# Optimization experiments

Hardware: AMD Instinct MI355X
Metric: run time of the kernel (lower is better)

The kernel has to match this reference:

```python
import jax, jax.numpy as jnp
import numpy as np

B = 16          # number of point clouds
N_COARSE = 1024  # points per cloud at coarse level
N_FINE = 4096    # points per cloud at fine level
C_IN = 256       # coarse feature channels
C_SKIP = 128     # fine skip feature channels
C_HID = 256
EPS = 1e-16


def setup_inputs() -> dict:
    key = jax.random.key(0)
    ks = jax.random.split(key, 8)
    x = jax.random.normal(ks[0], (B * N_COARSE, C_IN), dtype=jnp.float32)
    pos = jax.random.uniform(ks[1], (B * N_COARSE, 3), dtype=jnp.float32)
    x_skip = jax.random.normal(ks[2], (B * N_FINE, C_SKIP), dtype=jnp.float32)
    pos_skip = jax.random.uniform(ks[3], (B * N_FINE, 3), dtype=jnp.float32)
    # uniform batch assignment (sorted), one segment per cloud
    batch = jnp.repeat(jnp.arange(B, dtype=jnp.int32), N_COARSE)
    batch_skip = jnp.repeat(jnp.arange(B, dtype=jnp.int32), N_FINE)
    # MLP params: Linear(384 -> 256) + ReLU, Linear(256 -> 256) + ReLU
    c0 = C_IN + C_SKIP
    W1 = jax.random.normal(ks[4], (c0, C_HID), dtype=jnp.float32) / np.sqrt(c0)
    b1 = jnp.zeros((C_HID,), dtype=jnp.float32)
    W2 = jax.random.normal(ks[5], (C_HID, C_HID), dtype=jnp.float32) / np.sqrt(C_HID)
    b2 = jnp.zeros((C_HID,), dtype=jnp.float32)
    return {"x": x, "pos": pos, "x_skip": x_skip, "pos_skip": pos_skip,
            "W1": W1, "b1": b1, "W2": W2, "b2": b2,
            "batch": batch, "batch_skip": batch_skip, "k": 3}


def _knn_interpolate(x, pos, pos_skip, k):
    # batch is uniform: reshape into [B, n, ...] blocks (same as per-batch kNN)
    xb = x.reshape(B, N_COARSE, -1)          # [B, Nc, C]
    pc = pos.reshape(B, N_COARSE, 3)         # [B, Nc, 3]
    pf = pos_skip.reshape(B, N_FINE, 3)      # [B, Nf, 3]
    # squared pairwise distances within each cloud: [B, Nf, Nc]
    d2 = jnp.sum((pf[:, :, None, :] - pc[:, None, :, :]) ** 2, axis=-1)
    neg_d2, idx = jax.lax.top_k(-d2, k)      # k nearest -> [B, Nf, k]
    w = 1.0 / jnp.maximum(-neg_d2, EPS)      # inverse-squared-distance weights
    gathered = jax.vmap(lambda xc, i: xc[i])(xb, idx)  # [B, Nf, k, C]
    interp = jnp.sum(w[..., None] * gathered, axis=2) / jnp.sum(w, axis=2, keepdims=True)
    return interp.reshape(B * N_FINE, -1)    # [B*Nf, C]


def reference(x, pos, x_skip, pos_skip, W1, b1, W2, b2, batch, batch_skip, k):
    x_up = _knn_interpolate(x, pos, pos_skip, k)
    h = jnp.concatenate([x_up, x_skip], axis=1)          # [B*Nf, C_IN+C_SKIP]
    h = jax.nn.relu(h @ W1 + b1)
    h = jax.nn.relu(h @ W2 + b2)
    return (h, pos_skip, batch_skip)
```

## Files before the change

kernel.cpp:

```cpp
#include <hip/hip_runtime.h>

#define B_ 16
#define NC 1024
#define NF 4096
#define CIN 256
#define CSKIP 128
#define CHID 256
#define MTOT (B_ * NF)
#define EPS_ 1e-16f

typedef _Float16 f16;
typedef __attribute__((ext_vector_type(8))) _Float16 f16x8;
typedef __attribute__((ext_vector_type(4))) _Float16 f16x4;
typedef __attribute__((ext_vector_type(4))) float f32x4;


__global__ __launch_bounds__(256) void misc_kernel(
    const float* __restrict__ pos, const float* __restrict__ pos_skip,
    const int* __restrict__ batch_skip,
    const float* __restrict__ W1, const float* __restrict__ W2,
    const float* __restrict__ b1,
    int* __restrict__ idx3, float* __restrict__ w3,
    f16* __restrict__ W1aT, f16* __restrict__ W1bT, f16* __restrict__ W2T,
    float* __restrict__ b1p, float* __restrict__ out_tail)
{
    __shared__ float4 cpos[NC];
    __shared__ float  cd[32 * 24];
    __shared__ int    ci[32 * 24];

    const int bid = blockIdx.x;
    if (bid < 2048) {
        const int b  = bid >> 7;
        const int fb = bid & 127;
        const float* cp = pos + (size_t)b * NC * 3;
        for (int i = threadIdx.x; i < NC; i += 256)
            cpos[i] = make_float4(cp[i * 3], cp[i * 3 + 1], cp[i * 3 + 2], 0.0f);
        __syncthreads();

        const int fl = threadIdx.x & 31;
        const int q  = threadIdx.x >> 5;
        const int f  = b * NF + fb * 32 + fl;
        const float px = pos_skip[f * 3 + 0];
        const float py = pos_skip[f * 3 + 1];
        const float pz = pos_skip[f * 3 + 2];

        float d0 = 3.4e38f, d1 = 3.4e38f, d2 = 3.4e38f;
        int   i0 = 0, i1 = 0, i2 = 0;
        const int jbase = q << 7;
#pragma unroll 4
        for (int jj = 0; jj < 128; ++jj) {
            const int j = jbase + jj;
            float4 c = cpos[j];
            float dx = px - c.x, dy = py - c.y, dz = pz - c.z;
            float d = fmaf(dx, dx, fmaf(dy, dy, dz * dz));
            const bool c2 = d < d2, c1 = d < d1, c0 = d < d0;
            d2 = c1 ? d1 : (c2 ? d : d2);  i2 = c1 ? i1 : (c2 ? j : i2);
            d1 = c0 ? d0 : (c1 ? d : d1);  i1 = c0 ? i0 : (c1 ? j : i1);
            d0 = c0 ? d  : d0;             i0 = c0 ? j  : i0;
        }
        const int cb = fl * 24 + q * 3;
        cd[cb + 0] = d0; cd[cb + 1] = d1; cd[cb + 2] = d2;
        ci[cb + 0] = i0; ci[cb + 1] = i1; ci[cb + 2] = i2;
        __syncthreads();

        if (threadIdx.x < 32) {
            float e0 = 3.4e38f, e1 = 3.4e38f, e2 = 3.4e38f;
            int   j0 = 0, j1 = 0, j2 = 0;
#pragma unroll
            for (int s = 0; s < 24; ++s) {
                const float d = cd[fl * 24 + s];
                const int   j = ci[fl * 24 + s];
                const bool c2 = d < e2, c1 = d < e1, c0 = d < e0;
                e2 = c1 ? e1 : (c2 ? d : e2);  j2 = c1 ? j1 : (c2 ? j : j2);
                e1 = c0 ? e0 : (c1 ? d : e1);  j1 = c0 ? j0 : (c1 ? j : j1);
                e0 = c0 ? d  : e0;             j0 = c0 ? j  : j0;
            }
            const float w0 = 1.0f / fmaxf(e0, EPS_);
            const float w1 = 1.0f / fmaxf(e1, EPS_);
            const float w2 = 1.0f / fmaxf(e2, EPS_);
            const float inv = 1.0f / (w0 + w1 + w2);
            idx3[f * 3 + 0] = b * NC + j0;
            idx3[f * 3 + 1] = b * NC + j1;
            idx3[f * 3 + 2] = b * NC + j2;
            w3[f * 3 + 0] = w0 * inv;
            w3[f * 3 + 1] = w1 * inv;
            w3[f * 3 + 2] = w2 * inv;
        }
    } else if (bid < 2689) {
        const int t = (bid - 2048) * 256 + threadIdx.x;
        if (t < 256 * 256) {
            const int k = t >> 8, n = t & 255;
            W1aT[n * 256 + k] = (f16)W1[k * 256 + n];
        } else if (t < 256 * 256 + 128 * 256) {
            const int u = t - 256 * 256;
            const int k = u >> 8, n = u & 255;
            W1bT[n * 128 + k] = (f16)W1[(256 + k) * 256 + n];
        } else if (t < 256 * 256 + 128 * 256 + 256 * 256) {
            const int u = t - 256 * 256 - 128 * 256;
            const int n = u >> 8, j = u & 255;
            const int k = (j & ~63) + ((j & 3) << 4) + ((j >> 2) & 15);
            W2T[n * 256 + j] = (f16)W2[k * 256 + n];
        } else if (t < 256 * 256 + 128 * 256 + 256 * 256 + 256) {
            const int j = t - (256 * 256 + 128 * 256 + 256 * 256);
            const int k = (j & ~63) + ((j & 3) << 4) + ((j >> 2) & 15);
            b1p[j] = b1[k];
        }
    } else {
        const int i = (bid - 2689) * 256 + threadIdx.x;
        const int npos = MTOT * 3;
        if (i < npos)               out_tail[i] = pos_skip[i];
        else if (i < npos + MTOT)   out_tail[i] = (float)batch_skip[i - npos];
    }
}

__device__ __forceinline__ void gload16(const void* g, void* l)
{
    __builtin_amdgcn_global_load_lds(
        (const __attribute__((address_space(1))) unsigned int*)g,
        (__attribute__((address_space(3))) unsigned int*)l, 16, 0, 0);
}

__global__ __launch_bounds__(256, 2) void gemm_y(
    const float* __restrict__ A, const f16* __restrict__ Bt,
    f16* __restrict__ C)
{
    __shared__ f16 As[128 * 64];
    __shared__ f16 Bs[256 * 64];
    const int tid  = threadIdx.x;
    const int lane = tid & 63;
    const int wid  = tid >> 6;
    const int wr   = wid >> 1, wc = wid & 1;
    const int m0   = blockIdx.x * 128;

    const int srow = tid >> 1;
    const int scg  = tid & 1;
    const int srow_l = lane >> 3;
    const int kch    = (lane & 7) ^ ((lane >> 3) & 7);

    f32x4 acc[4][8] = {};

    for (int k0 = 0; k0 < 256; k0 += 64) {
#pragma unroll
        for (int r = 0; r < 8; ++r) {
            const int c = (wid << 3) + r;
            const int row = (c << 3) + srow_l;
            gload16(Bt + (size_t)row * 256 + k0 + kch * 8,
                    (char*)Bs + (c << 10));
        }
        {
            const float* p = A + (size_t)(m0 + srow) * 256 + k0 + scg * 32;
            float v[32];
#pragma unroll
            for (int j = 0; j < 8; ++j) {
                float4 a = ((const float4*)p)[j];
                v[j * 4 + 0] = a.x; v[j * 4 + 1] = a.y;
                v[j * 4 + 2] = a.z; v[j * 4 + 3] = a.w;
            }
#pragma unroll
            for (int j = 0; j < 4; ++j) {
                f16x8 hh;
#pragma unroll
                for (int t2 = 0; t2 < 8; ++t2) hh[t2] = (f16)v[j * 8 + t2];
                const int sphys = (scg * 4 + j) ^ (srow & 7);
                *(f16x8*)((char*)As + srow * 128 + sphys * 16) = hh;
            }
        }
        __syncthreads();

#pragma unroll
        for (int h = 0; h < 2; ++h) {
            f16x8 aF[4];
#pragma unroll
            for (int m = 0; m < 4; ++m) {
                const int row  = wr * 64 + m * 16 + (lane & 15);
                const int kg   = (h << 2) + (lane >> 4);
                const int slot = kg ^ (row & 7);
                aF[m] = *(const f16x8*)((const char*)As + row * 128 + slot * 16);
            }
#pragma unroll
            for (int n = 0; n < 8; ++n) {
                const int row  = wc * 128 + n * 16 + (lane & 15);
                const int kg   = (h << 2) + (lane >> 4);
                const int slot = kg ^ (row & 7);
                f16x8 bF = *(const f16x8*)((const char*)Bs + row * 128 + slot * 16);
#pragma unroll
                for (int m = 0; m < 4; ++m)
                    acc[m][n] = __builtin_amdgcn_mfma_f32_16x16x32_f16(
                        aF[m], bF, acc[m][n], 0, 0, 0);
            }
        }
        __syncthreads();
    }

    const int qq = lane & 15;
#pragma unroll
    for (int m = 0; m < 4; ++m) {
        const int rb = wr * 64 + m * 16 + ((lane >> 4) << 2);
#pragma unroll
        for (int r = 0; r < 4; ++r) {
            const int rg = m0 + rb + r;
#pragma unroll
            for (int g = 0; g < 2; ++g) {
                f16x4 hv;
#pragma unroll
                for (int n = 0; n < 4; ++n)
                    hv[n] = (f16)acc[m][g * 4 + n][r];
                *(f16x4*)&C[(size_t)rg * 256 + wc * 128 + g * 64 + qq * 4] = hv;
            }
        }
    }
}

__global__ __launch_bounds__(256, 2) void gemm1b_fused(
    const float* __restrict__ A, const f16* __restrict__ Bt,
    const f16* __restrict__ y,
    const int* __restrict__ idx3, const float* __restrict__ w3,
    const float* __restrict__ b1p, f16* __restrict__ h1)
{
    __shared__ f16 As[128 * 64];
    __shared__ f16 Bs[256 * 64];
    const int tid  = threadIdx.x;
    const int lane = tid & 63;
    const int wid  = tid >> 6;
    const int wr   = wid >> 1, wc = wid & 1;
    const int m0   = blockIdx.x * 128;

    const int srow = tid >> 1;
    const int scg  = tid & 1;
    const int srow_l = lane >> 3;
    const int kch    = (lane & 7) ^ ((lane >> 3) & 7);

    f32x4 acc[4][8] = {};

    for (int k0 = 0; k0 < 128; k0 += 64) {
#pragma unroll
        for (int r = 0; r < 8; ++r) {
            const int c = (wid << 3) + r;
            const int row = (c << 3) + srow_l;
            gload16(Bt + (size_t)row * 128 + k0 + kch * 8,
                    (char*)Bs + (c << 10));
        }
        {
            const float* p = A + (size_t)(m0 + srow) * 128 + k0 + scg * 32;
            float v[32];
#pragma unroll
            for (int j = 0; j < 8; ++j) {
                float4 a = ((const float4*)p)[j];
                v[j * 4 + 0] = a.x; v[j * 4 + 1] = a.y;
                v[j * 4 + 2] = a.z; v[j * 4 + 3] = a.w;
            }
#pragma unroll
            for (int j = 0; j < 4; ++j) {
                f16x8 hh;
#pragma unroll
                for (int t2 = 0; t2 < 8; ++t2) hh[t2] = (f16)v[j * 8 + t2];
                const int sphys = (scg * 4 + j) ^ (srow & 7);
                *(f16x8*)((char*)As + srow * 128 + sphys * 16) = hh;
            }
        }
        __syncthreads();

#pragma unroll
        for (int h = 0; h < 2; ++h) {
            f16x8 aF[4];
#pragma unroll
            for (int m = 0; m < 4; ++m) {
                const int row  = wr * 64 + m * 16 + (lane & 15);
                const int kg   = (h << 2) + (lane >> 4);
                const int slot = kg ^ (row & 7);
                aF[m] = *(const f16x8*)((const char*)As + row * 128 + slot * 16);
            }
#pragma unroll
            for (int n = 0; n < 8; ++n) {
                const int row  = wc * 128 + n * 16 + (lane & 15);
                const int kg   = (h << 2) + (lane >> 4);
                const int slot = kg ^ (row & 7);
                f16x8 bF = *(const f16x8*)((const char*)Bs + row * 128 + slot * 16);
#pragma unroll
                for (int m = 0; m < 4; ++m)
                    acc[m][n] = __builtin_amdgcn_mfma_f32_16x16x32_f16(
                        aF[m], bF, acc[m][n], 0, 0, 0);
            }
        }
        __syncthreads();
    }

    const int qq = lane & 15;
    const f32x4 bv0 = *(const f32x4*)&b1p[wc * 128 + qq * 4];
    const f32x4 bv1 = *(const f32x4*)&b1p[wc * 128 + 64 + qq * 4];
#pragma unroll
    for (int m = 0; m < 4; ++m) {
        const int rb = wr * 64 + m * 16 + ((lane >> 4) << 2);
#pragma unroll
        for (int r = 0; r < 4; ++r) {
            const int rg = m0 + rb + r;
            const int i0 = idx3[rg * 3 + 0], i1 = idx3[rg * 3 + 1], i2 = idx3[rg * 3 + 2];
            const float w0 = w3[rg * 3 + 0], w1 = w3[rg * 3 + 1], w2 = w3[rg * 3 + 2];
#pragma unroll
            for (int g = 0; g < 2; ++g) {
                const int jb = wc * 128 + g * 64 + qq * 4;
                f16x4 y0 = *(const f16x4*)&y[(size_t)i0 * 256 + jb];
                f16x4 y1 = *(const f16x4*)&y[(size_t)i1 * 256 + jb];
                f16x4 y2 = *(const f16x4*)&y[(size_t)i2 * 256 + jb];
                const f32x4 bv = g ? bv1 : bv0;
                f16x4 hv;
#pragma unroll
                for (int n = 0; n < 4; ++n) {
                    float v = acc[m][g * 4 + n][r]
                            + w0 * (float)y0[n] + w1 * (float)y1[n] + w2 * (float)y2[n]
                            + bv[n];
                    hv[n] = (f16)fmaxf(v, 0.0f);
                }
                *(f16x4*)&h1[(size_t)rg * 256 + jb] = hv;
            }
        }
    }
}

__global__ __launch_bounds__(256, 2) void gemm2_kernel(
    const f16* __restrict__ A, const f16* __restrict__ Bt,
    const float* __restrict__ bias, float* __restrict__ out)
{
    __shared__ f16 As[128 * 64];
    __shared__ f16 Bs[256 * 64];
    const int tid  = threadIdx.x;
    const int lane = tid & 63;
    const int wid  = tid >> 6;
    const int wr   = wid >> 1, wc = wid & 1;
    const int m0   = blockIdx.x * 128;

    const int srow_l = lane >> 3;
    const int kch    = (lane & 7) ^ ((lane >> 3) & 7);

    f32x4 acc[4][8] = {};

    for (int k0 = 0; k0 < 256; k0 += 64) {
#pragma unroll
        for (int r = 0; r < 4; ++r) {
            const int c = (wid << 2) + r;
            const int row = (c << 3) + srow_l;
            gload16(A + (size_t)(m0 + row) * 256 + k0 + kch * 8,
                    (char*)As + (c << 10));
        }
#pragma unroll
        for (int r = 0; r < 8; ++r) {
            const int c = (wid << 3) + r;
            const int row = (c << 3) + srow_l;
            gload16(Bt + (size_t)row * 256 + k0 + kch * 8,
                    (char*)Bs + (c << 10));
        }
        __syncthreads();

#pragma unroll
        for (int h = 0; h < 2; ++h) {
            f16x8 aF[4];
#pragma unroll
            for (int m = 0; m < 4; ++m) {
                const int row  = wr * 64 + m * 16 + (lane & 15);
                const int kg   = (h << 2) + (lane >> 4);
                const int slot = kg ^ (row & 7);
                aF[m] = *(const f16x8*)((const char*)As + row * 128 + slot * 16);
            }
#pragma unroll
            for (int n = 0; n < 8; ++n) {
                const int row  = wc * 128 + n * 16 + (lane & 15);
                const int kg   = (h << 2) + (lane >> 4);
                const int slot = kg ^ (row & 7);
                f16x8 bF = *(const f16x8*)((const char*)Bs + row * 128 + slot * 16);
#pragma unroll
                for (int m = 0; m < 4; ++m)
                    acc[m][n] = __builtin_amdgcn_mfma_f32_16x16x32_f16(
                        aF[m], bF, acc[m][n], 0, 0, 0);
            }
        }
        __syncthreads();
    }

#pragma unroll
    for (int m = 0; m < 4; ++m) {
#pragma unroll
        for (int n = 0; n < 8; ++n) {
            const int col = wc * 128 + n * 16 + (lane & 15);
            const float bv = bias[col];
#pragma unroll
            for (int r = 0; r < 4; ++r) {
                const int row = m0 + wr * 64 + m * 16 + ((lane >> 4) << 2) + r;
                out[(size_t)row * 256 + col] = fmaxf(acc[m][n][r] + bv, 0.0f);
            }
        }
    }
}

extern "C" void kernel_launch(void* const* d_in, const int* in_sizes, int n_in,
                              void* d_out, int out_size, void* d_ws, size_t ws_size,
                              hipStream_t stream)
{
    const float* x        = (const float*)d_in[0];
    const float* pos      = (const float*)d_in[1];
    const float* x_skip   = (const float*)d_in[2];
    const float* pos_skip = (const float*)d_in[3];
    const float* W1       = (const float*)d_in[4];
    const float* b1       = (const float*)d_in[5];
    const float* W2       = (const float*)d_in[6];
    const float* b2       = (const float*)d_in[7];
    const int*   batch_skip = (const int*)d_in[9];
    float* out = (float*)d_out;

    char* ws = (char*)d_ws;
    int*   idx3  = (int*)ws;
    float* w3    = (float*)(ws + (1u << 20));
    f16*   W1aT  = (f16*)(ws + (2u << 20));
    f16*   W1bT  = (f16*)(ws + (2u << 20) + (256u << 10));
    f16*   W2T   = (f16*)(ws + (2u << 20) + (512u << 10));
    float* b1p   = (float*)(ws + (2u << 20) + (768u << 10));
    f16*   y     = (f16*)(ws + (4u << 20));
    f16*   h1    = (f16*)(ws + (16u << 20));

    misc_kernel<<<3713, 256, 0, stream>>>(
        pos, pos_skip, batch_skip, W1, W2, b1,
        idx3, w3, W1aT, W1bT, W2T, b1p, out + (size_t)MTOT * CHID);

    gemm_y<<<B_ * NC / 128, 256, 0, stream>>>(x, W1aT, y);

    gemm1b_fused<<<MTOT / 128, 256, 0, stream>>>(x_skip, W1bT, y, idx3, w3, b1p, h1);

    gemm2_kernel<<<MTOT / 128, 256, 0, stream>>>(h1, W2T, b2, out);
}
```

Measured before the change: 198.5 us.

## Fuse GEMM1b and GEMM2 via LDS-resident h1; fold y GEMM into misc kernel

```diff
diff --git a/kernel.cpp b/kernel.cpp
--- a/kernel.cpp
+++ b/kernel.cpp
@@ -15,34 +15,137 @@
 typedef __attribute__((ext_vector_type(4))) float f32x4;
 
 
-__global__ __launch_bounds__(256) void misc_kernel(
+__device__ __forceinline__ void gload16(const void* g, void* l)
+{
+    __builtin_amdgcn_global_load_lds(
+        (const __attribute__((address_space(1))) unsigned int*)g,
+        (__attribute__((address_space(3))) unsigned int*)l, 16, 0, 0);
+}
+
+__global__ __launch_bounds__(256, 4) void misc_kernel(
+    const float* __restrict__ x,
     const float* __restrict__ pos, const float* __restrict__ pos_skip,
     const int* __restrict__ batch_skip,
     const float* __restrict__ W1, const float* __restrict__ W2,
     const float* __restrict__ b1,
     int* __restrict__ idx3, float* __restrict__ w3,
-    f16* __restrict__ W1aT, f16* __restrict__ W1bT, f16* __restrict__ W2T,
-    float* __restrict__ b1p, float* __restrict__ out_tail)
+    f16* __restrict__ W1bT, f16* __restrict__ W2T, float* __restrict__ b1p,
+    f16* __restrict__ y, float* __restrict__ out_tail)
 {
-    __shared__ float4 cpos[NC];
-    __shared__ float  cd[32 * 24];
-    __shared__ int    ci[32 * 24];
-
+    __shared__ __align__(16) char smem[32768];
     const int bid = blockIdx.x;
-    if (bid < 2048) {
-        const int b  = bid >> 7;
-        const int fb = bid & 127;
+
+    if (bid < 256) {
+        f16* As = (f16*)smem;
+        f16* Bs = (f16*)(smem + 16384);
+        const int m0 = (bid >> 1) * 128;
+        const int n0 = (bid & 1) * 128;
+        const int tid  = threadIdx.x;
+        const int lane = tid & 63;
+        const int wid  = tid >> 6;
+        const int wr   = wid >> 1, wc = wid & 1;
+        const int srow = tid >> 1;
+        const int scg  = tid & 1;
+        const int bn4  = (tid & 31) << 2;
+        const int bkb  = (tid >> 5) << 3;
+
+        f32x4 acc[4][4] = {};
+        for (int k0 = 0; k0 < 256; k0 += 64) {
+            {
+                const float* p = x + (size_t)(m0 + srow) * 256 + k0 + scg * 32;
+                float v[32];
+#pragma unroll
+                for (int j = 0; j < 8; ++j) {
+                    float4 a = ((const float4*)p)[j];
+                    v[j*4+0]=a.x; v[j*4+1]=a.y; v[j*4+2]=a.z; v[j*4+3]=a.w;
+                }
+#pragma unroll
+                for (int j = 0; j < 4; ++j) {
+                    f16x8 hh;
+#pragma unroll
+                    for (int t2 = 0; t2 < 8; ++t2) hh[t2] = (f16)v[j*8+t2];
+                    const int sphys = (scg*4 + j) ^ (srow & 7);
+                    *(f16x8*)((char*)As + srow*128 + sphys*16) = hh;
+                }
+            }
+#pragma unroll
+            for (int c = 0; c < 2; ++c) {
+                const int k = bkb + c * 4;
+                const float* wp = W1 + (size_t)(k0 + k) * 256 + n0 + bn4;
+                float4 r0 = *(const float4*)(wp);
+                float4 r1 = *(const float4*)(wp + 256);
+                float4 r2 = *(const float4*)(wp + 512);
+                float4 r3 = *(const float4*)(wp + 768);
+                const int half  = (k >> 2) & 1;
+                const int kslot = k >> 3;
+                f16x4 t0, t1, t2v, t3;
+                t0[0]=(f16)r0.x; t0[1]=(f16)r1.x; t0[2]=(f16)r2.x; t0[3]=(f16)r3.x;
+                t1[0]=(f16)r0.y; t1[1]=(f16)r1.y; t1[2]=(f16)r2.y; t1[3]=(f16)r3.y;
+                t2v[0]=(f16)r0.z; t2v[1]=(f16)r1.z; t2v[2]=(f16)r2.z; t2v[3]=(f16)r3.z;
+                t3[0]=(f16)r0.w; t3[1]=(f16)r1.w; t3[2]=(f16)r2.w; t3[3]=(f16)r3.w;
+                *(f16x4*)((char*)Bs + (bn4+0)*128 + ((kslot ^ ((bn4+0)&7))*16) + half*8) = t0;
+                *(f16x4*)((char*)Bs + (bn4+1)*128 + ((kslot ^ ((bn4+1)&7))*16) + half*8) = t1;
+                *(f16x4*)((char*)Bs + (bn4+2)*128 + ((kslot ^ ((bn4+2)&7))*16) + half*8) = t2v;
+                *(f16x4*)((char*)Bs + (bn4+3)*128 + ((kslot ^ ((bn4+3)&7))*16) + half*8) = t3;
+            }
+            __syncthreads();
+#pragma unroll
+            for (int h = 0; h < 2; ++h) {
+                f16x8 aF[4], bF[4];
+#pragma unroll
+                for (int m = 0; m < 4; ++m) {
+                    const int row  = wr*64 + m*16 + (lane & 15);
+                    const int kg   = (h<<2) + (lane>>4);
+                    const int slot = kg ^ (row & 7);
+                    aF[m] = *(const f16x8*)((const char*)As + row*128 + slot*16);
+                }
+#pragma unroll
+                for (int n = 0; n < 4; ++n) {
+                    const int row  = wc*64 + n*16 + (lane & 15);
+                    const int kg   = (h<<2) + (lane>>4);
+                    const int slot = kg ^ (row & 7);
+                    bF[n] = *(const f16x8*)((const char*)Bs + row*128 + slot*16);
+                }
+#pragma unroll
+                for (int m = 0; m < 4; ++m)
+#pragma unroll
+                    for (int n = 0; n < 4; ++n)
+                        acc[m][n] = __builtin_amdgcn_mfma_f32_16x16x32_f16(
+                            aF[m], bF[n], acc[m][n], 0, 0, 0);
+            }
+            __syncthreads();
+        }
+        const int qq = lane & 15;
+#pragma unroll
+        for (int m = 0; m < 4; ++m) {
+            const int rb = wr*64 + m*16 + ((lane>>4) << 2);
+#pragma unroll
+            for (int r = 0; r < 4; ++r) {
+                const int rg = m0 + rb + r;
+                f16x4 hv;
+#pragma unroll
+                for (int n = 0; n < 4; ++n) hv[n] = (f16)acc[m][n][r];
+                *(f16x4*)&y[(size_t)rg * 256 + n0 + wc*64 + qq*4] = hv;
+            }
+        }
+    } else if (bid < 2304) {
+        float4* cpos = (float4*)smem;
+        float*  cd   = (float*)(smem + 16384);
+        int*    ci   = (int*)(smem + 19456);
+        const int kb = bid - 256;
+        const int b  = kb >> 7;
+        const int fb = kb & 127;
         const float* cp = pos + (size_t)b * NC * 3;
         for (int i = threadIdx.x; i < NC; i += 256)
-            cpos[i] = make_float4(cp[i * 3], cp[i * 3 + 1], cp[i * 3 + 2], 0.0f);
+            cpos[i] = make_float4(cp[i*3], cp[i*3+1], cp[i*3+2], 0.0f);
         __syncthreads();
 
         const int fl = threadIdx.x & 31;
         const int q  = threadIdx.x >> 5;
         const int f  = b * NF + fb * 32 + fl;
-        const float px = pos_skip[f * 3 + 0];
-        const float py = pos_skip[f * 3 + 1];
-        const float pz = pos_skip[f * 3 + 2];
+        const float px = pos_skip[f*3+0];
+        const float py = pos_skip[f*3+1];
+        const float pz = pos_skip[f*3+2];
 
         float d0 = 3.4e38f, d1 = 3.4e38f, d2 = 3.4e38f;
         int   i0 = 0, i1 = 0, i2 = 0;
@@ -59,8 +162,8 @@
             d0 = c0 ? d  : d0;             i0 = c0 ? j  : i0;
         }
         const int cb = fl * 24 + q * 3;
-        cd[cb + 0] = d0; cd[cb + 1] = d1; cd[cb + 2] = d2;
-        ci[cb + 0] = i0; ci[cb + 1] = i1; ci[cb + 2] = i2;
+        cd[cb+0] = d0; cd[cb+1] = d1; cd[cb+2] = d2;
+        ci[cb+0] = i0; ci[cb+1] = i1; ci[cb+2] = i2;
         __syncthreads();
 
         if (threadIdx.x < 32) {
@@ -68,8 +171,8 @@
             int   j0 = 0, j1 = 0, j2 = 0;
 #pragma unroll
             for (int s = 0; s < 24; ++s) {
-                const float d = cd[fl * 24 + s];
-                const int   j = ci[fl * 24 + s];
+                const float d = cd[fl*24 + s];
+                const int   j = ci[fl*24 + s];
                 const bool c2 = d < e2, c1 = d < e1, c0 = d < e0;
                 e2 = c1 ? e1 : (c2 ? d : e2);  j2 = c1 ? j1 : (c2 ? j : j2);
                 e1 = c0 ? e0 : (c1 ? d : e1);  j1 = c0 ? j0 : (c1 ? j : j1);
@@ -79,29 +182,25 @@
             const float w1 = 1.0f / fmaxf(e1, EPS_);
             const float w2 = 1.0f / fmaxf(e2, EPS_);
             const float inv = 1.0f / (w0 + w1 + w2);
-            idx3[f * 3 + 0] = b * NC + j0;
-            idx3[f * 3 + 1] = b * NC + j1;
-            idx3[f * 3 + 2] = b * NC + j2;
-            w3[f * 3 + 0] = w0 * inv;
-            w3[f * 3 + 1] = w1 * inv;
-            w3[f * 3 + 2] = w2 * inv;
+            idx3[f*3+0] = b * NC + j0;
+            idx3[f*3+1] = b * NC + j1;
+            idx3[f*3+2] = b * NC + j2;
+            w3[f*3+0] = w0 * inv;
+            w3[f*3+1] = w1 * inv;
+            w3[f*3+2] = w2 * inv;
         }
     } else if (bid < 2689) {
-        const int t = (bid - 2048) * 256 + threadIdx.x;
-        if (t < 256 * 256) {
+        const int t = (bid - 2304) * 256 + threadIdx.x;
+        if (t < 128 * 256) {
             const int k = t >> 8, n = t & 255;
-            W1aT[n * 256 + k] = (f16)W1[k * 256 + n];
-        } else if (t < 256 * 256 + 128 * 256) {
-            const int u = t - 256 * 256;
-            const int k = u >> 8, n = u & 255;
             W1bT[n * 128 + k] = (f16)W1[(256 + k) * 256 + n];
-        } else if (t < 256 * 256 + 128 * 256 + 256 * 256) {
-            const int u = t - 256 * 256 - 128 * 256;
+        } else if (t < 128 * 256 + 256 * 256) {
+            const int u = t - 128 * 256;
             const int n = u >> 8, j = u & 255;
             const int k = (j & ~63) + ((j & 3) << 4) + ((j >> 2) & 15);
             W2T[n * 256 + j] = (f16)W2[k * 256 + n];
-        } else if (t < 256 * 256 + 128 * 256 + 256 * 256 + 256) {
-            const int j = t - (256 * 256 + 128 * 256 + 256 * 256);
+        } else if (t < 128 * 256 + 256 * 256 + 256) {
+            const int j = t - (128 * 256 + 256 * 256);
             const int k = (j & ~63) + ((j & 3) << 4) + ((j >> 2) & 15);
             b1p[j] = b1[k];
         }
@@ -113,78 +212,75 @@
     }
 }
 
-__device__ __forceinline__ void gload16(const void* g, void* l)
+__global__ __launch_bounds__(256, 2) void fused_gemm12(
+    const float* __restrict__ A,
+    const f16* __restrict__ B1t,
+    const f16* __restrict__ y,
+    const int* __restrict__ idx3, const float* __restrict__ w3,
+    const float* __restrict__ b1p,
+    const f16* __restrict__ B2t,
+    const float* __restrict__ b2,
+    float* __restrict__ out)
 {
-    __builtin_amdgcn_global_load_lds(
-        (const __attribute__((address_space(1))) unsigned int*)g,
-        (__attribute__((address_space(3))) unsigned int*)l, 16, 0, 0);
-}
-
-__global__ __launch_bounds__(256, 2) void gemm_y(
-    const float* __restrict__ A, const f16* __restrict__ Bt,
-    f16* __restrict__ C)
-{
-    __shared__ f16 As[128 * 64];
-    __shared__ f16 Bs[256 * 64];
+    __shared__ __align__(16) char lds[65536];
+    f16*  Bs  = (f16*)lds;
+    f16*  As  = (f16*)(lds + 32768);
+    char* h1s = lds + 32768;
+
     const int tid  = threadIdx.x;
     const int lane = tid & 63;
     const int wid  = tid >> 6;
     const int wr   = wid >> 1, wc = wid & 1;
-    const int m0   = blockIdx.x * 128;
-
-    const int srow = tid >> 1;
-    const int scg  = tid & 1;
+    const int m0   = blockIdx.x * 64;
+
     const int srow_l = lane >> 3;
     const int kch    = (lane & 7) ^ ((lane >> 3) & 7);
 
-    f32x4 acc[4][8] = {};
-
-    for (int k0 = 0; k0 < 256; k0 += 64) {
+    f32x4 acc[2][8] = {};
+    for (int k0 = 0; k0 < 128; k0 += 64) {
 #pragma unroll
         for (int r = 0; r < 8; ++r) {
             const int c = (wid << 3) + r;
             const int row = (c << 3) + srow_l;
-            gload16(Bt + (size_t)row * 256 + k0 + kch * 8,
-                    (char*)Bs + (c << 10));
+            gload16(B1t + (size_t)row * 128 + k0 + kch * 8, (char*)Bs + (c << 10));
         }
         {
-            const float* p = A + (size_t)(m0 + srow) * 256 + k0 + scg * 32;
-            float v[32];
-#pragma unroll
-            for (int j = 0; j < 8; ++j) {
+            const int arow = tid >> 2, acg = tid & 3;
+            const float* p = A + (size_t)(m0 + arow) * 128 + k0 + acg * 16;
+            float v[16];
+#pragma unroll
+            for (int j = 0; j < 4; ++j) {
                 float4 a = ((const float4*)p)[j];
-                v[j * 4 + 0] = a.x; v[j * 4 + 1] = a.y;
-                v[j * 4 + 2] = a.z; v[j * 4 + 3] = a.w;
-            }
-#pragma unroll
-            for (int j = 0; j < 4; ++j) {
+                v[j*4+0]=a.x; v[j*4+1]=a.y; v[j*4+2]=a.z; v[j*4+3]=a.w;
+            }
+#pragma unroll
+            for (int j = 0; j < 2; ++j) {
                 f16x8 hh;
 #pragma unroll
-                for (int t2 = 0; t2 < 8; ++t2) hh[t2] = (f16)v[j * 8 + t2];
-                const int sphys = (scg * 4 + j) ^ (srow & 7);
-                *(f16x8*)((char*)As + srow * 128 + sphys * 16) = hh;
-            }
-        }
-        __syncthreads();
-
+                for (int t2 = 0; t2 < 8; ++t2) hh[t2] = (f16)v[j*8+t2];
+                const int sphys = (acg*2 + j) ^ (arow & 7);
+                *(f16x8*)((char*)As + arow*128 + sphys*16) = hh;
+            }
+        }
+        __syncthreads();
 #pragma unroll
         for (int h = 0; h < 2; ++h) {
-            f16x8 aF[4];
-#pragma unroll
-            for (int m = 0; m < 4; ++m) {
-                const int row  = wr * 64 + m * 16 + (lane & 15);
-                const int kg   = (h << 2) + (lane >> 4);
+            f16x8 aF[2];
+#pragma unroll
+            for (int m = 0; m < 2; ++m) {
+                const int row  = wr*32 + m*16 + (lane & 15);
+                const int kg   = (h<<2) + (lane>>4);
                 const int slot = kg ^ (row & 7);
-                aF[m] = *(const f16x8*)((const char*)As + row * 128 + slot * 16);
+                aF[m] = *(const f16x8*)((const char*)As + row*128 + slot*16);
             }
 #pragma unroll
             for (int n = 0; n < 8; ++n) {
-                const int row  = wc * 128 + n * 16 + (lane & 15);
-                const int kg   = (h << 2) + (lane >> 4);
+                const int row  = wc*128 + n*16 + (lane & 15);
+                const int kg   = (h<<2) + (lane>>4);
                 const int slot = kg ^ (row & 7);
-                f16x8 bF = *(const f16x8*)((const char*)Bs + row * 128 + slot * 16);
-#pragma unroll
-                for (int m = 0; m < 4; ++m)
+                f16x8 bF = *(const f16x8*)((const char*)Bs + row*128 + slot*16);
+#pragma unroll
+                for (int m = 0; m < 2; ++m)
                     acc[m][n] = __builtin_amdgcn_mfma_f32_16x16x32_f16(
                         aF[m], bF, acc[m][n], 0, 0, 0);
             }
@@ -193,112 +289,20 @@
     }
 
     const int qq = lane & 15;
-#pragma unroll
-    for (int m = 0; m < 4; ++m) {
-        const int rb = wr * 64 + m * 16 + ((lane >> 4) << 2);
+    const f32x4 bv0 = *(const f32x4*)&b1p[wc*128 + qq*4];
+    const f32x4 bv1 = *(const f32x4*)&b1p[wc*128 + 64 + qq*4];
+#pragma unroll
+    for (int m = 0; m < 2; ++m) {
+        const int rb = wr*32 + m*16 + ((lane>>4) << 2);
 #pragma unroll
         for (int r = 0; r < 4; ++r) {
-            const int rg = m0 + rb + r;
+            const int rl = rb + r;
+            const int rg = m0 + rl;
+            const int i0 = idx3[rg*3+0], i1 = idx3[rg*3+1], i2 = idx3[rg*3+2];
+            const float w0 = w3[rg*3+0], w1 = w3[rg*3+1], w2 = w3[rg*3+2];
 #pragma unroll
             for (int g = 0; g < 2; ++g) {
-                f16x4 hv;
-#pragma unroll
-                for (int n = 0; n < 4; ++n)
-                    hv[n] = (f16)acc[m][g * 4 + n][r];
-                *(f16x4*)&C[(size_t)rg * 256 + wc * 128 + g * 64 + qq * 4] = hv;
-            }
-        }
-    }
-}
-
-__global__ __launch_bounds__(256, 2) void gemm1b_fused(
-    const float* __restrict__ A, const f16* __restrict__ Bt,
-    const f16* __restrict__ y,
-    const int* __restrict__ idx3, const float* __restrict__ w3,
-    const float* __restrict__ b1p, f16* __restrict__ h1)
-{
-    __shared__ f16 As[128 * 64];
-    __shared__ f16 Bs[256 * 64];
-    const int tid  = threadIdx.x;
-    const int lane = tid & 63;
-    const int wid  = tid >> 6;
-    const int wr   = wid >> 1, wc = wid & 1;
-    const int m0   = blockIdx.x * 128;
-
-    const int srow = tid >> 1;
-    const int scg  = tid & 1;
-    const int srow_l = lane >> 3;
-    const int kch    = (lane & 7) ^ ((lane >> 3) & 7);
-
-    f32x4 acc[4][8] = {};
-
-    for (int k0 = 0; k0 < 128; k0 += 64) {
-#pragma unroll
-        for (int r = 0; r < 8; ++r) {
-            const int c = (wid << 3) + r;
-            const int row = (c << 3) + srow_l;
-            gload16(Bt + (size_t)row * 128 + k0 + kch * 8,
-                    (char*)Bs + (c << 10));
-        }
-        {
-            const float* p = A + (size_t)(m0 + srow) * 128 + k0 + scg * 32;
-            float v[32];
-#pragma unroll
-            for (int j = 0; j < 8; ++j) {
-                float4 a = ((const float4*)p)[j];
-                v[j * 4 + 0] = a.x; v[j * 4 + 1] = a.y;
-                v[j * 4 + 2] = a.z; v[j * 4 + 3] = a.w;
-            }
-#pragma unroll
-            for (int j = 0; j < 4; ++j) {
-                f16x8 hh;
-#pragma unroll
-                for (int t2 = 0; t2 < 8; ++t2) hh[t2] = (f16)v[j * 8 + t2];
-                const int sphys = (scg * 4 + j) ^ (srow & 7);
-                *(f16x8*)((char*)As + srow * 128 + sphys * 16) = hh;
-            }
-        }
-        __syncthreads();
-
-#pragma unroll
-        for (int h = 0; h < 2; ++h) {
-            f16x8 aF[4];
-#pragma unroll
-            for (int m = 0; m < 4; ++m) {
-                const int row  = wr * 64 + m * 16 + (lane & 15);
-                const int kg   = (h << 2) + (lane >> 4);
-                const int slot = kg ^ (row & 7);
-                aF[m] = *(const f16x8*)((const char*)As + row * 128 + slot * 16);
-            }
-#pragma unroll
-            for (int n = 0; n < 8; ++n) {
-                const int row  = wc * 128 + n * 16 + (lane & 15);
-                const int kg   = (h << 2) + (lane >> 4);
-                const int slot = kg ^ (row & 7);
-                f16x8 bF = *(const f16x8*)((const char*)Bs + row * 128 + slot * 16);
-#pragma unroll
-                for (int m = 0; m < 4; ++m)
-                    acc[m][n] = __builtin_amdgcn_mfma_f32_16x16x32_f16(
-                        aF[m], bF, acc[m][n], 0, 0, 0);
-            }
-        }
-        __syncthreads();
-    }
-
-    const int qq = lane & 15;
-    const f32x4 bv0 = *(const f32x4*)&b1p[wc * 128 + qq * 4];
-    const f32x4 bv1 = *(const f32x4*)&b1p[wc * 128 + 64 + qq * 4];
-#pragma unroll
-    for (int m = 0; m < 4; ++m) {
-        const int rb = wr * 64 + m * 16 + ((lane >> 4) << 2);
-#pragma unroll
-        for (int r = 0; r < 4; ++r) {
-            const int rg = m0 + rb + r;
-            const int i0 = idx3[rg * 3 + 0], i1 = idx3[rg * 3 + 1], i2 = idx3[rg * 3 + 2];
-            const float w0 = w3[rg * 3 + 0], w1 = w3[rg * 3 + 1], w2 = w3[rg * 3 + 2];
-#pragma unroll
-            for (int g = 0; g < 2; ++g) {
-                const int jb = wc * 128 + g * 64 + qq * 4;
+                const int jb = wc*128 + g*64 + qq*4;
                 f16x4 y0 = *(const f16x4*)&y[(size_t)i0 * 256 + jb];
                 f16x4 y1 = *(const f16x4*)&y[(size_t)i1 * 256 + jb];
                 f16x4 y2 = *(const f16x4*)&y[(size_t)i2 * 256 + jb];
@@ -306,86 +310,63 @@
                 f16x4 hv;
 #pragma unroll
                 for (int n = 0; n < 4; ++n) {
-                    float v = acc[m][g * 4 + n][r]
-                            + w0 * (float)y0[n] + w1 * (float)y1[n] + w2 * (float)y2[n]
+                    float v = acc[m][g*4+n][r]
+                            + w0*(float)y0[n] + w1*(float)y1[n] + w2*(float)y2[n]
                             + bv[n];
                     hv[n] = (f16)fmaxf(v, 0.0f);
                 }
-                *(f16x4*)&h1[(size_t)rg * 256 + jb] = hv;
+                const int slot = jb >> 3;
+                const int phys = (slot & ~7) | ((slot & 7) ^ (rl & 7));
+                *(f16x4*)(h1s + rl*512 + phys*16 + ((jb >> 2) & 1) * 8) = hv;
             }
         }
     }
-}
-
-__global__ __launch_bounds__(256, 2) void gemm2_kernel(
-    const f16* __restrict__ A, const f16* __restrict__ Bt,
-    const float* __restrict__ bias, float* __restrict__ out)
-{
-    __shared__ f16 As[128 * 64];
-    __shared__ f16 Bs[256 * 64];
-    const int tid  = threadIdx.x;
-    const int lane = tid & 63;
-    const int wid  = tid >> 6;
-    const int wr   = wid >> 1, wc = wid & 1;
-    const int m0   = blockIdx.x * 128;
-
-    const int srow_l = lane >> 3;
-    const int kch    = (lane & 7) ^ ((lane >> 3) & 7);
-
-    f32x4 acc[4][8] = {};
-
+    __syncthreads();
+
+    f32x4 acc2[2][8] = {};
     for (int k0 = 0; k0 < 256; k0 += 64) {
-#pragma unroll
-        for (int r = 0; r < 4; ++r) {
-            const int c = (wid << 2) + r;
-            const int row = (c << 3) + srow_l;
-            gload16(A + (size_t)(m0 + row) * 256 + k0 + kch * 8,
-                    (char*)As + (c << 10));
-        }
 #pragma unroll
         for (int r = 0; r < 8; ++r) {
             const int c = (wid << 3) + r;
             const int row = (c << 3) + srow_l;
-            gload16(Bt + (size_t)row * 256 + k0 + kch * 8,
-                    (char*)Bs + (c << 10));
-        }
-        __syncthreads();
-
+            gload16(B2t + (size_t)row * 256 + k0 + kch * 8, (char*)Bs + (c << 10));
+        }
+        __syncthreads();
 #pragma unroll
         for (int h = 0; h < 2; ++h) {
-            f16x8 aF[4];
-#pragma unroll
-            for (int m = 0; m < 4; ++m) {
-                const int row  = wr * 64 + m * 16 + (lane & 15);
-                const int kg   = (h << 2) + (lane >> 4);
+            f16x8 aF[2];
+#pragma unroll
+            for (int m = 0; m < 2; ++m) {
+                const int row   = wr*32 + m*16 + (lane & 15);
+                const int kg    = (h<<2) + (lane>>4);
+                const int aslot = (k0 >> 3) + (kg ^ (row & 7));
+                aF[m] = *(const f16x8*)(h1s + row*512 + aslot*16);
+            }
+#pragma unroll
+            for (int n = 0; n < 8; ++n) {
+                const int row  = wc*128 + n*16 + (lane & 15);
+                const int kg   = (h<<2) + (lane>>4);
                 const int slot = kg ^ (row & 7);
-                aF[m] = *(const f16x8*)((const char*)As + row * 128 + slot * 16);
-            }
-#pragma unroll
-            for (int n = 0; n < 8; ++n) {
-                const int row  = wc * 128 + n * 16 + (lane & 15);
-                const int kg   = (h << 2) + (lane >> 4);
-                const int slot = kg ^ (row & 7);
-                f16x8 bF = *(const f16x8*)((const char*)Bs + row * 128 + slot * 16);
-#pragma unroll
-                for (int m = 0; m < 4; ++m)
-                    acc[m][n] = __builtin_amdgcn_mfma_f32_16x16x32_f16(
-                        aF[m], bF, acc[m][n], 0, 0, 0);
+                f16x8 bF = *(const f16x8*)((const char*)Bs + row*128 + slot*16);
+#pragma unroll
+                for (int m = 0; m < 2; ++m)
+                    acc2[m][n] = __builtin_amdgcn_mfma_f32_16x16x32_f16(
+                        aF[m], bF, acc2[m][n], 0, 0, 0);
             }
         }
         __syncthreads();
     }
 
 #pragma unroll
-    for (int m = 0; m < 4; ++m) {
+    for (int m = 0; m < 2; ++m) {
 #pragma unroll
         for (int n = 0; n < 8; ++n) {
-            const int col = wc * 128 + n * 16 + (lane & 15);
-            const float bv = bias[col];
+            const int col = wc*128 + n*16 + (lane & 15);
+            const float bv = b2[col];
 #pragma unroll
             for (int r = 0; r < 4; ++r) {
-                const int row = m0 + wr * 64 + m * 16 + ((lane >> 4) << 2) + r;
-                out[(size_t)row * 256 + col] = fmaxf(acc[m][n][r] + bv, 0.0f);
+                const int row = m0 + wr*32 + m*16 + ((lane>>4) << 2) + r;
+                out[(size_t)row * 256 + col] = fmaxf(acc2[m][n][r] + bv, 0.0f);
             }
         }
     }
@@ -407,22 +388,17 @@
     float* out = (float*)d_out;
 
     char* ws = (char*)d_ws;
-    int*   idx3  = (int*)ws;
-    float* w3    = (float*)(ws + (1u << 20));
-    f16*   W1aT  = (f16*)(ws + (2u << 20));
-    f16*   W1bT  = (f16*)(ws + (2u << 20) + (256u << 10));
-    f16*   W2T   = (f16*)(ws + (2u << 20) + (512u << 10));
-    float* b1p   = (float*)(ws + (2u << 20) + (768u << 10));
-    f16*   y     = (f16*)(ws + (4u << 20));
-    f16*   h1    = (f16*)(ws + (16u << 20));
+    int*   idx3 = (int*)ws;
+    float* w3   = (float*)(ws + (1u << 20));
+    f16*   W1bT = (f16*)(ws + (2u << 20));
+    f16*   W2T  = (f16*)(ws + (2u << 20) + (256u << 10));
+    float* b1p  = (float*)(ws + (2u << 20) + (512u << 10));
+    f16*   y    = (f16*)(ws + (4u << 20));
 
     misc_kernel<<<3713, 256, 0, stream>>>(
-        pos, pos_skip, batch_skip, W1, W2, b1,
-        idx3, w3, W1aT, W1bT, W2T, b1p, out + (size_t)MTOT * CHID);
-
-    gemm_y<<<B_ * NC / 128, 256, 0, stream>>>(x, W1aT, y);
-
-    gemm1b_fused<<<MTOT / 128, 256, 0, stream>>>(x_skip, W1bT, y, idx3, w3, b1p, h1);
-
-    gemm2_kernel<<<MTOT / 128, 256, 0, stream>>>(h1, W2T, b2, out);
+        x, pos, pos_skip, batch_skip, W1, W2, b1,
+        idx3, w3, W1bT, W2T, b1p, y, out + (size_t)MTOT * CHID);
+
+    fused_gemm12<<<MTOT / 64, 256, 0, stream>>>(
+        x_skip, W1bT, y, idx3, w3, b1p, W2T, b2, out);
 }
```

Result: faster. 177.7 us (-10.5%).
